# Performance work log

Measured on AMD Instinct MI355X. Metric: run time of the kernel, lower is better.

## Reference

```python
import jax, jax.numpy as jnp
import numpy as np

H, W = 8, 64
HK, WK = 7, 11
N = H * W            # 512 tokens
C = 512              # embed_dim
HEADS = 8
HD = C // HEADS      # 64
SCALE = HD ** -0.5
B = 32


def build_local_mask():
    # Faithful port of the build() mask construction.
    m = np.ones([N, H + HK - 1, W + WK - 1], dtype=np.int32)
    for h in range(H):
        for w in range(W):
            m[h * W + w, h:h + HK, w:w + WK] = 0
    m = m[:, HK // 2:H + HK // 2, WK // 2:W + WK // 2].reshape(-1, N).astype(bool)
    mask = np.where(m, -1e30, 0.0).astype(np.float32)
    return jnp.asarray(mask.reshape(1, 1, N, N))


def setup_inputs() -> dict:
    key = jax.random.key(0)
    k1, k2, k3, k4 = jax.random.split(key, 4)
    return {
        "x": jax.random.normal(k1, (B, N, C), dtype=jnp.float32),
        "w_qkv": jax.random.normal(k2, (C, 3 * C), dtype=jnp.float32) * (C ** -0.5),
        "w_proj": jax.random.normal(k3, (C, C), dtype=jnp.float32) * (C ** -0.5),
        "b_proj": jax.random.normal(k4, (C,), dtype=jnp.float32) * 0.01,
        "mask": build_local_mask(),
    }


def reference(x, w_qkv, w_proj, b_proj, mask):
    b = x.shape[0]
    qkv = x @ w_qkv                                   # [B, N, 3C]
    qkv = qkv.reshape(b, N, 3, HEADS, HD)
    qkv = jnp.transpose(qkv, (2, 0, 3, 1, 4))          # [3, B, heads, N, hd]
    q, k, v = qkv[0], qkv[1], qkv[2]
    attn = jnp.einsum("bhnd,bhmd->bhnm", q * SCALE, k) + mask  # [B, heads, N, N]
    attn = jax.nn.softmax(attn, axis=-1)
    out = jnp.einsum("bhnm,bhmd->bhnd", attn, v)       # [B, heads, N, hd]
    out = jnp.transpose(out, (0, 2, 1, 3)).reshape(b, N, C)
    return out @ w_proj + b_proj
```

## Files before the change

kernel.cpp:

```cpp
#include <hip/hip_runtime.h>
#include <hip/hip_bf16.h>

typedef __attribute__((ext_vector_type(8))) __bf16 bf16x8;
typedef __attribute__((ext_vector_type(4))) float f32x4;

__device__ __forceinline__ unsigned short f2bf(float f) {
    unsigned int u = __float_as_uint(f);
    unsigned int r = u + 0x7FFFu + ((u >> 16) & 1u);
    return (unsigned short)(r >> 16);
}

__device__ __forceinline__ void async_copy16(const unsigned short* g, unsigned short* l) {
    __builtin_amdgcn_global_load_lds(
        (__attribute__((address_space(1))) void*)(g),
        (__attribute__((address_space(3))) void*)(l), 16, 0, 0);
}

__global__ __launch_bounds__(256) void cvt_f32_bf16(const float4* __restrict__ in,
                                                    uint4* __restrict__ out, int n8) {
    int i = blockIdx.x * blockDim.x + threadIdx.x;
    if (i >= n8) return;
    float4 a = in[2 * i], b = in[2 * i + 1];
    union { unsigned short s[8]; uint4 v; } r;
    r.s[0] = f2bf(a.x); r.s[1] = f2bf(a.y); r.s[2] = f2bf(a.z); r.s[3] = f2bf(a.w);
    r.s[4] = f2bf(b.x); r.s[5] = f2bf(b.y); r.s[6] = f2bf(b.z); r.s[7] = f2bf(b.w);
    out[i] = r.v;
}

__global__ __launch_bounds__(256) void transpose_cvt(const float* __restrict__ in,
                                                     unsigned short* __restrict__ out,
                                                     int R, int C) {
    __shared__ float tile[32][33];
    int c0 = blockIdx.x * 32, r0 = blockIdx.y * 32;
    int tx = threadIdx.x, ty = threadIdx.y;
    #pragma unroll
    for (int i = 0; i < 32; i += 8)
        tile[ty + i][tx] = in[(size_t)(r0 + ty + i) * C + c0 + tx];
    __syncthreads();
    #pragma unroll
    for (int i = 0; i < 32; i += 8)
        out[(size_t)(c0 + ty + i) * R + r0 + tx] = f2bf(tile[tx][ty + i]);
}

__device__ __forceinline__ void gemm_core_128(const unsigned short* __restrict__ A,
                                              const unsigned short* __restrict__ Bt,
                                              int K, int m0, int n0, f32x4 acc[4][4]) {
    __shared__ unsigned short As[128 * 64];
    __shared__ unsigned short Bs[128 * 64];
    const int lane = threadIdx.x & 63;
    const int wv   = threadIdx.x >> 6;
    const int wm = (wv >> 1) * 64, wn = (wv & 1) * 64;
    const int l15 = lane & 15, l16 = lane >> 4;

    f32x4 zz = {0.f, 0.f, 0.f, 0.f};
    #pragma unroll
    for (int i = 0; i < 4; ++i)
        #pragma unroll
        for (int j = 0; j < 4; ++j) acc[i][j] = zz;

    for (int k0 = 0; k0 < K; k0 += 64) {
        if (k0) __syncthreads();
        #pragma unroll
        for (int c = 0; c < 4; ++c) {
            int flat16 = c * 256 + (int)threadIdx.x;
            int r  = flat16 >> 3;
            int kk = (flat16 & 7) * 8;
            async_copy16(A  + (size_t)(m0 + r) * K + k0 + kk, As + flat16 * 8);
            async_copy16(Bt + (size_t)(n0 + r) * K + k0 + kk, Bs + flat16 * 8);
        }
        __syncthreads();
        #pragma unroll
        for (int kk = 0; kk < 64; kk += 32) {
            bf16x8 a[4], b[4];
            #pragma unroll
            for (int i = 0; i < 4; ++i)
                a[i] = *(const bf16x8*)(const void*)(As + (wm + i * 16 + l15) * 64 + kk + l16 * 8);
            #pragma unroll
            for (int i = 0; i < 4; ++i)
                b[i] = *(const bf16x8*)(const void*)(Bs + (wn + i * 16 + l15) * 64 + kk + l16 * 8);
            #pragma unroll
            for (int i = 0; i < 4; ++i)
                #pragma unroll
                for (int j = 0; j < 4; ++j)
                    acc[i][j] = __builtin_amdgcn_mfma_f32_16x16x32_bf16(a[i], b[j], acc[i][j], 0, 0, 0);
        }
    }
}

__global__ __launch_bounds__(256) void gemm_qkv(const unsigned short* __restrict__ xb,
                                                const unsigned short* __restrict__ wT,
                                                unsigned short* __restrict__ Qb,
                                                unsigned short* __restrict__ Kb,
                                                unsigned short* __restrict__ Vb) {
    f32x4 acc[4][4];
    int m0 = blockIdx.y * 128, n0 = blockIdx.x * 128;
    gemm_core_128(xb, wT, 512, m0, n0, acc);
    const int lane = threadIdx.x & 63, wv = threadIdx.x >> 6;
    const int wm = (wv >> 1) * 64, wn = (wv & 1) * 64;
    const int l15 = lane & 15, l16 = lane >> 4;
    #pragma unroll
    for (int j = 0; j < 4; ++j) {
        int col = n0 + wn + j * 16 + l15;
        int t = col >> 9;
        int within = col & 511;
        int h = within >> 6, d = within & 63;
        unsigned short* dst = (t == 0) ? Qb : (t == 1) ? Kb : Vb;
        float scl = (t == 0) ? 0.125f : 1.0f;
        #pragma unroll
        for (int i = 0; i < 4; ++i)
            #pragma unroll
            for (int e = 0; e < 4; ++e) {
                int row = m0 + wm + i * 16 + (l16 << 2) + e;
                int b = row >> 9, n = row & 511;
                dst[(((size_t)b * 8 + h) * 512 + n) * 64 + d] = f2bf(acc[i][j][e] * scl);
            }
    }
}

__global__ __launch_bounds__(256) void attn_kernel(const unsigned short* __restrict__ Qb,
                                                   const unsigned short* __restrict__ Kb,
                                                   const unsigned short* __restrict__ Vb,
                                                   unsigned short* __restrict__ Ob) {
    __shared__ unsigned short Ks[128 * 72];
    __shared__ unsigned short Vt[64 * 136];
    __shared__ unsigned short Ps[4 * 32 * 136];

    const int bh = blockIdx.x >> 2;
    const int qt = blockIdx.x & 3;
    const int lane = threadIdx.x & 63;
    const int wv = threadIdx.x >> 6;
    const int l15 = lane & 15, l16 = lane >> 4;
    const int b = bh >> 3, h = bh & 7;

    const unsigned short* Qp = Qb + (size_t)bh * 512 * 64;
    const unsigned short* Kp = Kb + (size_t)bh * 512 * 64;
    const unsigned short* Vp = Vb + (size_t)bh * 512 * 64;
    unsigned short* Pw = Ps + wv * 32 * 136;

    const int qrow0 = qt * 128 + wv * 32;

    bf16x8 aQ[2][2];
    #pragma unroll
    for (int mf = 0; mf < 2; ++mf)
        #pragma unroll
        for (int kf = 0; kf < 2; ++kf)
            aQ[mf][kf] = *(const bf16x8*)(const void*)(Qp + (size_t)(qrow0 + mf * 16 + l15) * 64 + kf * 32 + l16 * 8);

    f32x4 o[2][4];
    f32x4 zz = {0.f, 0.f, 0.f, 0.f};
    float mrow[2][4], lrow[2][4];
    #pragma unroll
    for (int mf = 0; mf < 2; ++mf) {
        #pragma unroll
        for (int df = 0; df < 4; ++df) o[mf][df] = zz;
        #pragma unroll
        for (int j = 0; j < 4; ++j) { mrow[mf][j] = -INFINITY; lrow[mf][j] = 0.f; }
    }

    for (int kt = 0; kt < 4; ++kt) {
        if (((kt > qt) ? (kt - qt) : (qt - kt)) >= 3) continue;
        __syncthreads();
        #pragma unroll
        for (int c = 0; c < 4; ++c) {
            int flat16 = c * 256 + (int)threadIdx.x;
            int key = flat16 >> 3, d = (flat16 & 7) * 8;
            *(uint4*)(Ks + key * 72 + d) = *(const uint4*)(Kp + (size_t)(kt * 128 + key) * 64 + d);
        }
        #pragma unroll
        for (int c = 0; c < 4; ++c) {
            int flat16 = c * 256 + (int)threadIdx.x;
            int key = flat16 & 127, dc = flat16 >> 7;
            union { uint4 v; unsigned short s[8]; } t;
            t.v = *(const uint4*)(Vp + (size_t)(kt * 128 + key) * 64 + dc * 8);
            #pragma unroll
            for (int e = 0; e < 8; ++e) Vt[(dc * 8 + e) * 136 + key] = t.s[e];
        }
        __syncthreads();

        f32x4 s[2][8];
        #pragma unroll
        for (int mf = 0; mf < 2; ++mf)
            #pragma unroll
            for (int nf = 0; nf < 8; ++nf) s[mf][nf] = zz;
        #pragma unroll
        for (int nf = 0; nf < 8; ++nf) {
            bf16x8 bk0 = *(const bf16x8*)(const void*)(Ks + (nf * 16 + l15) * 72 + 0  + l16 * 8);
            bf16x8 bk1 = *(const bf16x8*)(const void*)(Ks + (nf * 16 + l15) * 72 + 32 + l16 * 8);
            #pragma unroll
            for (int mf = 0; mf < 2; ++mf) {
                s[mf][nf] = __builtin_amdgcn_mfma_f32_16x16x32_bf16(aQ[mf][0], bk0, s[mf][nf], 0, 0, 0);
                s[mf][nf] = __builtin_amdgcn_mfma_f32_16x16x32_bf16(aQ[mf][1], bk1, s[mf][nf], 0, 0, 0);
            }
        }

        float tmax[2][4];
        #pragma unroll
        for (int mf = 0; mf < 2; ++mf)
            #pragma unroll
            for (int j = 0; j < 4; ++j) tmax[mf][j] = -INFINITY;
        #pragma unroll
        for (int mf = 0; mf < 2; ++mf)
            #pragma unroll
            for (int nf = 0; nf < 8; ++nf) {
                int key = kt * 128 + nf * 16 + l15;
                int kh = key >> 6, kw = key & 63;
                #pragma unroll
                for (int j = 0; j < 4; ++j) {
                    int q = qrow0 + mf * 16 + (l16 << 2) + j;
                    int qh = q >> 6, qw = q & 63;
                    int dh = qh - kh; dh = dh < 0 ? -dh : dh;
                    int dw = qw - kw; dw = dw < 0 ? -dw : dw;
                    float v = (dh <= 3 && dw <= 5) ? s[mf][nf][j] : -1e30f;
                    s[mf][nf][j] = v;
                    tmax[mf][j] = fmaxf(tmax[mf][j], v);
                }
            }
        #pragma unroll
        for (int mf = 0; mf < 2; ++mf)
            #pragma unroll
            for (int j = 0; j < 4; ++j) {
                float t = tmax[mf][j];
                t = fmaxf(t, __shfl_xor(t, 1));
                t = fmaxf(t, __shfl_xor(t, 2));
                t = fmaxf(t, __shfl_xor(t, 4));
                t = fmaxf(t, __shfl_xor(t, 8));
                tmax[mf][j] = t;
            }
        float fscale[2][4];
        #pragma unroll
        for (int mf = 0; mf < 2; ++mf)
            #pragma unroll
            for (int j = 0; j < 4; ++j) {
                float mnew = fmaxf(mrow[mf][j], tmax[mf][j]);
                fscale[mf][j] = __expf(mrow[mf][j] - mnew);
                mrow[mf][j] = mnew;
                lrow[mf][j] *= fscale[mf][j];
            }
        #pragma unroll
        for (int mf = 0; mf < 2; ++mf)
            #pragma unroll
            for (int df = 0; df < 4; ++df)
                #pragma unroll
                for (int j = 0; j < 4; ++j) o[mf][df][j] *= fscale[mf][j];

        #pragma unroll
        for (int mf = 0; mf < 2; ++mf) {
            float lsum[4] = {0.f, 0.f, 0.f, 0.f};
            #pragma unroll
            for (int nf = 0; nf < 8; ++nf) {
                #pragma unroll
                for (int j = 0; j < 4; ++j) {
                    float p = __expf(s[mf][nf][j] - mrow[mf][j]);
                    lsum[j] += p;
                    Pw[(mf * 16 + (l16 << 2) + j) * 136 + nf * 16 + l15] = f2bf(p);
                }
            }
            #pragma unroll
            for (int j = 0; j < 4; ++j) {
                float t = lsum[j];
                t += __shfl_xor(t, 1); t += __shfl_xor(t, 2);
                t += __shfl_xor(t, 4); t += __shfl_xor(t, 8);
                lrow[mf][j] += t;
            }
        }
        __syncthreads();

        #pragma unroll
        for (int kf = 0; kf < 4; ++kf) {
            bf16x8 aP[2];
            #pragma unroll
            for (int mf = 0; mf < 2; ++mf)
                aP[mf] = *(const bf16x8*)(const void*)(Pw + (mf * 16 + l15) * 136 + kf * 32 + l16 * 8);
            #pragma unroll
            for (int df = 0; df < 4; ++df) {
                bf16x8 bV = *(const bf16x8*)(const void*)(Vt + (df * 16 + l15) * 136 + kf * 32 + l16 * 8);
                #pragma unroll
                for (int mf = 0; mf < 2; ++mf)
                    o[mf][df] = __builtin_amdgcn_mfma_f32_16x16x32_bf16(aP[mf], bV, o[mf][df], 0, 0, 0);
            }
        }
    }

    #pragma unroll
    for (int mf = 0; mf < 2; ++mf)
        #pragma unroll
        for (int j = 0; j < 4; ++j) {
            float inv = 1.0f / lrow[mf][j];
            int q = qrow0 + mf * 16 + (l16 << 2) + j;
            size_t base = ((size_t)b * 512 + q) * 512 + h * 64;
            #pragma unroll
            for (int df = 0; df < 4; ++df)
                Ob[base + df * 16 + l15] = f2bf(o[mf][df][j] * inv);
        }
}

__global__ __launch_bounds__(256) void gemm_proj(const unsigned short* __restrict__ Ab,
                                                 const unsigned short* __restrict__ wT,
                                                 const float* __restrict__ bias,
                                                 float* __restrict__ out) {
    f32x4 acc[4][4];
    int m0 = blockIdx.y * 128, n0 = blockIdx.x * 128;
    gemm_core_128(Ab, wT, 512, m0, n0, acc);
    const int lane = threadIdx.x & 63, wv = threadIdx.x >> 6;
    const int wm = (wv >> 1) * 64, wn = (wv & 1) * 64;
    const int l15 = lane & 15, l16 = lane >> 4;
    #pragma unroll
    for (int j = 0; j < 4; ++j) {
        int col = n0 + wn + j * 16 + l15;
        float bb = bias[col];
        #pragma unroll
        for (int i = 0; i < 4; ++i)
            #pragma unroll
            for (int e = 0; e < 4; ++e) {
                int row = m0 + wm + i * 16 + (l16 << 2) + e;
                out[(size_t)row * 512 + col] = acc[i][j][e] + bb;
            }
    }
}

extern "C" void kernel_launch(void* const* d_in, const int* in_sizes, int n_in,
                              void* d_out, int out_size, void* d_ws, size_t ws_size,
                              hipStream_t stream) {
    const float* x      = (const float*)d_in[0];
    const float* w_qkv  = (const float*)d_in[1];
    const float* w_proj = (const float*)d_in[2];
    const float* b_proj = (const float*)d_in[3];
    float* out = (float*)d_out;

    char* ws = (char*)d_ws;
    unsigned short* xb     = (unsigned short*)(ws);
    unsigned short* wqkvT  = (unsigned short*)(ws + 16777216);
    unsigned short* wprojT = (unsigned short*)(ws + 18350080);
    unsigned short* Qb     = (unsigned short*)(ws + 18874368);
    unsigned short* Kb     = (unsigned short*)(ws + 35651584);
    unsigned short* Vb     = (unsigned short*)(ws + 52428800);
    unsigned short* Ob     = xb;

    cvt_f32_bf16<<<4096, 256, 0, stream>>>((const float4*)x, (uint4*)xb, 1048576);
    transpose_cvt<<<dim3(48, 16), dim3(32, 8), 0, stream>>>(w_qkv, wqkvT, 512, 1536);
    transpose_cvt<<<dim3(16, 16), dim3(32, 8), 0, stream>>>(w_proj, wprojT, 512, 512);
    gemm_qkv<<<dim3(12, 128), 256, 0, stream>>>(xb, wqkvT, Qb, Kb, Vb);
    attn_kernel<<<1024, 256, 0, stream>>>(Qb, Kb, Vb, Ob);
    gemm_proj<<<dim3(4, 128), 256, 0, stream>>>(Ob, wprojT, b_proj, out);
}
```

Before: 124.2 us.

## Restructure local attention into per-image-row key tiles with transposed S and dead-block skipping

The attention kernel now walks key tiles of one image row (64 keys) instead of 128-key tiles. It skips rows farther than 3 from the warp's query row, and skips 16-key column groups that are fully outside the 11-wide window. S is computed transposed (K as the A operand) so each lane owns one query column. This lets the window mask be precomputed as a per-lane bitmask and cuts the row reductions to two cross-lane shuffles. P is packed with v_cvt_pk_bf16_f32 into per-wave LDS, the block barrier before PV is replaced by a compiler fence, LDS is reduced, and occupancy is hinted at 4 blocks per CU. The risks are per-wave LDS ordering subtleties and extra shuffles to redistribute the rescale factors.

```diff
diff --git a/kernel.cpp b/kernel.cpp
--- a/kernel.cpp
+++ b/kernel.cpp
@@ -117,181 +117,189 @@
     }
 }
 
-__global__ __launch_bounds__(256) void attn_kernel(const unsigned short* __restrict__ Qb,
-                                                   const unsigned short* __restrict__ Kb,
-                                                   const unsigned short* __restrict__ Vb,
-                                                   unsigned short* __restrict__ Ob) {
-    __shared__ unsigned short Ks[128 * 72];
-    __shared__ unsigned short Vt[64 * 136];
-    __shared__ unsigned short Ps[4 * 32 * 136];
+__global__ __launch_bounds__(256, 4) void attn_kernel(const unsigned short* __restrict__ Qb,
+                                                      const unsigned short* __restrict__ Kb,
+                                                      const unsigned short* __restrict__ Vb,
+                                                      unsigned short* __restrict__ Ob) {
+    __shared__ unsigned short Ks[64 * 72];
+    __shared__ unsigned short Vt[64 * 72];
+    __shared__ unsigned short Ps[4 * 32 * 72];
 
     const int bh = blockIdx.x >> 2;
     const int qt = blockIdx.x & 3;
-    const int lane = threadIdx.x & 63;
-    const int wv = threadIdx.x >> 6;
+    const int tid = threadIdx.x;
+    const int lane = tid & 63;
+    const int wv = tid >> 6;
     const int l15 = lane & 15, l16 = lane >> 4;
     const int b = bh >> 3, h = bh & 7;
 
     const unsigned short* Qp = Qb + (size_t)bh * 512 * 64;
     const unsigned short* Kp = Kb + (size_t)bh * 512 * 64;
     const unsigned short* Vp = Vb + (size_t)bh * 512 * 64;
-    unsigned short* Pw = Ps + wv * 32 * 136;
+    unsigned short* Pw = Ps + wv * 32 * 72;
 
     const int qrow0 = qt * 128 + wv * 32;
-
-    bf16x8 aQ[2][2];
-    #pragma unroll
-    for (int mf = 0; mf < 2; ++mf)
+    const int qh = qrow0 >> 6;
+    const int wq0 = qrow0 & 63;
+    const int dead_g = wq0 ? 0 : 3;
+
+    unsigned int wbits = 0;
+    {
+        int qw[2] = { wq0 + l15, wq0 + 16 + l15 };
+        #pragma unroll
+        for (int qf = 0; qf < 2; ++qf)
+            #pragma unroll
+            for (int g = 0; g < 4; ++g)
+                #pragma unroll
+                for (int j = 0; j < 4; ++j) {
+                    int kw = g * 16 + (l16 << 2) + j;
+                    int dw = qw[qf] - kw; dw = dw < 0 ? -dw : dw;
+                    wbits |= (dw <= 5 ? 1u : 0u) << (qf * 16 + g * 4 + j);
+                }
+    }
+
+    bf16x8 bQ[2][2];
+    #pragma unroll
+    for (int qf = 0; qf < 2; ++qf)
         #pragma unroll
         for (int kf = 0; kf < 2; ++kf)
-            aQ[mf][kf] = *(const bf16x8*)(const void*)(Qp + (size_t)(qrow0 + mf * 16 + l15) * 64 + kf * 32 + l16 * 8);
+            bQ[qf][kf] = *(const bf16x8*)(const void*)(Qp + (size_t)(qrow0 + qf * 16 + l15) * 64 + kf * 32 + l16 * 8);
 
     f32x4 o[2][4];
     f32x4 zz = {0.f, 0.f, 0.f, 0.f};
-    float mrow[2][4], lrow[2][4];
-    #pragma unroll
-    for (int mf = 0; mf < 2; ++mf) {
-        #pragma unroll
-        for (int df = 0; df < 4; ++df) o[mf][df] = zz;
-        #pragma unroll
-        for (int j = 0; j < 4; ++j) { mrow[mf][j] = -INFINITY; lrow[mf][j] = 0.f; }
-    }
-
-    for (int kt = 0; kt < 4; ++kt) {
-        if (((kt > qt) ? (kt - qt) : (qt - kt)) >= 3) continue;
+    float mrow[2] = {-INFINITY, -INFINITY}, lrow[2] = {0.f, 0.f};
+    #pragma unroll
+    for (int qf = 0; qf < 2; ++qf)
+        #pragma unroll
+        for (int df = 0; df < 4; ++df) o[qf][df] = zz;
+
+    for (int kh = 0; kh < 8; ++kh) {
+        int dlo = kh - 2 * qt;
+        if (dlo < -3 || dlo > 4) continue;
         __syncthreads();
         #pragma unroll
-        for (int c = 0; c < 4; ++c) {
-            int flat16 = c * 256 + (int)threadIdx.x;
-            int key = flat16 >> 3, d = (flat16 & 7) * 8;
-            *(uint4*)(Ks + key * 72 + d) = *(const uint4*)(Kp + (size_t)(kt * 128 + key) * 64 + d);
-        }
-        #pragma unroll
-        for (int c = 0; c < 4; ++c) {
-            int flat16 = c * 256 + (int)threadIdx.x;
-            int key = flat16 & 127, dc = flat16 >> 7;
+        for (int c = 0; c < 2; ++c) {
+            int flat16 = c * 256 + tid;
+            int key = flat16 >> 3, dk = (flat16 & 7) * 8;
+            *(uint4*)(void*)(Ks + key * 72 + dk) = *(const uint4*)(const void*)(Kp + ((size_t)(kh * 64 + key) * 64 + dk));
+        }
+        #pragma unroll
+        for (int c = 0; c < 2; ++c) {
+            int flat16 = c * 256 + tid;
+            int key = flat16 & 63, d8 = flat16 >> 6;
             union { uint4 v; unsigned short s[8]; } t;
-            t.v = *(const uint4*)(Vp + (size_t)(kt * 128 + key) * 64 + dc * 8);
-            #pragma unroll
-            for (int e = 0; e < 8; ++e) Vt[(dc * 8 + e) * 136 + key] = t.s[e];
+            t.v = *(const uint4*)(const void*)(Vp + ((size_t)(kh * 64 + key) * 64 + d8 * 8));
+            #pragma unroll
+            for (int e = 0; e < 8; ++e) Vt[(d8 * 8 + e) * 72 + key] = t.s[e];
         }
         __syncthreads();
 
-        f32x4 s[2][8];
-        #pragma unroll
-        for (int mf = 0; mf < 2; ++mf)
-            #pragma unroll
-            for (int nf = 0; nf < 8; ++nf) s[mf][nf] = zz;
-        #pragma unroll
-        for (int nf = 0; nf < 8; ++nf) {
-            bf16x8 bk0 = *(const bf16x8*)(const void*)(Ks + (nf * 16 + l15) * 72 + 0  + l16 * 8);
-            bf16x8 bk1 = *(const bf16x8*)(const void*)(Ks + (nf * 16 + l15) * 72 + 32 + l16 * 8);
-            #pragma unroll
-            for (int mf = 0; mf < 2; ++mf) {
-                s[mf][nf] = __builtin_amdgcn_mfma_f32_16x16x32_bf16(aQ[mf][0], bk0, s[mf][nf], 0, 0, 0);
-                s[mf][nf] = __builtin_amdgcn_mfma_f32_16x16x32_bf16(aQ[mf][1], bk1, s[mf][nf], 0, 0, 0);
-            }
-        }
-
-        float tmax[2][4];
-        #pragma unroll
-        for (int mf = 0; mf < 2; ++mf)
-            #pragma unroll
-            for (int j = 0; j < 4; ++j) tmax[mf][j] = -INFINITY;
-        #pragma unroll
-        for (int mf = 0; mf < 2; ++mf)
-            #pragma unroll
-            for (int nf = 0; nf < 8; ++nf) {
-                int key = kt * 128 + nf * 16 + l15;
-                int kh = key >> 6, kw = key & 63;
+        int adq = qh - kh; adq = adq < 0 ? -adq : adq;
+        if (adq > 3) continue;
+
+        f32x4 s[2][4];
+        #pragma unroll
+        for (int qf = 0; qf < 2; ++qf)
+            #pragma unroll
+            for (int g = 0; g < 4; ++g) s[qf][g] = zz;
+        #pragma unroll
+        for (int g = 0; g < 4; ++g) {
+            if (g == dead_g) continue;
+            bf16x8 aK0 = *(const bf16x8*)(const void*)(Ks + (g * 16 + l15) * 72 + 0  + l16 * 8);
+            bf16x8 aK1 = *(const bf16x8*)(const void*)(Ks + (g * 16 + l15) * 72 + 32 + l16 * 8);
+            #pragma unroll
+            for (int qf = 0; qf < 2; ++qf) {
+                s[qf][g] = __builtin_amdgcn_mfma_f32_16x16x32_bf16(aK0, bQ[qf][0], s[qf][g], 0, 0, 0);
+                s[qf][g] = __builtin_amdgcn_mfma_f32_16x16x32_bf16(aK1, bQ[qf][1], s[qf][g], 0, 0, 0);
+            }
+        }
+
+        float tmax[2] = {-1e30f, -1e30f};
+        #pragma unroll
+        for (int qf = 0; qf < 2; ++qf) {
+            #pragma unroll
+            for (int g = 0; g < 4; ++g) {
+                if (g == dead_g) continue;
                 #pragma unroll
                 for (int j = 0; j < 4; ++j) {
-                    int q = qrow0 + mf * 16 + (l16 << 2) + j;
-                    int qh = q >> 6, qw = q & 63;
-                    int dh = qh - kh; dh = dh < 0 ? -dh : dh;
-                    int dw = qw - kw; dw = dw < 0 ? -dw : dw;
-                    float v = (dh <= 3 && dw <= 5) ? s[mf][nf][j] : -1e30f;
-                    s[mf][nf][j] = v;
-                    tmax[mf][j] = fmaxf(tmax[mf][j], v);
+                    float v = ((wbits >> (qf * 16 + g * 4 + j)) & 1u) ? s[qf][g][j] : -1e30f;
+                    s[qf][g][j] = v;
+                    tmax[qf] = fmaxf(tmax[qf], v);
                 }
             }
-        #pragma unroll
-        for (int mf = 0; mf < 2; ++mf)
+            float t = tmax[qf];
+            t = fmaxf(t, __shfl_xor(t, 16));
+            t = fmaxf(t, __shfl_xor(t, 32));
+            tmax[qf] = t;
+        }
+
+        #pragma unroll
+        for (int qf = 0; qf < 2; ++qf) {
+            float mnew = fmaxf(mrow[qf], tmax[qf]);
+            float fs = __expf(mrow[qf] - mnew);
+            mrow[qf] = mnew;
+            lrow[qf] *= fs;
             #pragma unroll
             for (int j = 0; j < 4; ++j) {
-                float t = tmax[mf][j];
-                t = fmaxf(t, __shfl_xor(t, 1));
-                t = fmaxf(t, __shfl_xor(t, 2));
-                t = fmaxf(t, __shfl_xor(t, 4));
-                t = fmaxf(t, __shfl_xor(t, 8));
-                tmax[mf][j] = t;
-            }
-        float fscale[2][4];
-        #pragma unroll
-        for (int mf = 0; mf < 2; ++mf)
-            #pragma unroll
-            for (int j = 0; j < 4; ++j) {
-                float mnew = fmaxf(mrow[mf][j], tmax[mf][j]);
-                fscale[mf][j] = __expf(mrow[mf][j] - mnew);
-                mrow[mf][j] = mnew;
-                lrow[mf][j] *= fscale[mf][j];
-            }
-        #pragma unroll
-        for (int mf = 0; mf < 2; ++mf)
+                float fso = __shfl(fs, (l16 << 2) + j);
+                #pragma unroll
+                for (int df = 0; df < 4; ++df) o[qf][df][j] *= fso;
+            }
+        }
+
+        #pragma unroll
+        for (int qf = 0; qf < 2; ++qf) {
+            float lsum = 0.f;
+            #pragma unroll
+            for (int g = 0; g < 4; ++g) {
+                unsigned int lo, hi;
+                if (g == dead_g) {
+                    lo = 0u; hi = 0u;
+                } else {
+                    float e0 = __expf(s[qf][g][0] - mrow[qf]);
+                    float e1 = __expf(s[qf][g][1] - mrow[qf]);
+                    float e2 = __expf(s[qf][g][2] - mrow[qf]);
+                    float e3 = __expf(s[qf][g][3] - mrow[qf]);
+                    lsum += (e0 + e1) + (e2 + e3);
+                    asm("v_cvt_pk_bf16_f32 %0, %1, %2" : "=v"(lo) : "v"(e0), "v"(e1));
+                    asm("v_cvt_pk_bf16_f32 %0, %1, %2" : "=v"(hi) : "v"(e2), "v"(e3));
+                }
+                uint2 w; w.x = lo; w.y = hi;
+                *(uint2*)(void*)(Pw + (qf * 16 + l15) * 72 + g * 16 + (l16 << 2)) = w;
+            }
+            float t = lsum;
+            t += __shfl_xor(t, 16);
+            t += __shfl_xor(t, 32);
+            lrow[qf] += t;
+        }
+        asm volatile("" ::: "memory");
+
+        #pragma unroll
+        for (int kf = 0; kf < 2; ++kf) {
+            bf16x8 aP0 = *(const bf16x8*)(const void*)(Pw + (0 * 16 + l15) * 72 + kf * 32 + l16 * 8);
+            bf16x8 aP1 = *(const bf16x8*)(const void*)(Pw + (1 * 16 + l15) * 72 + kf * 32 + l16 * 8);
+            #pragma unroll
+            for (int df = 0; df < 4; ++df) {
+                bf16x8 bV = *(const bf16x8*)(const void*)(Vt + (df * 16 + l15) * 72 + kf * 32 + l16 * 8);
+                o[0][df] = __builtin_amdgcn_mfma_f32_16x16x32_bf16(aP0, bV, o[0][df], 0, 0, 0);
+                o[1][df] = __builtin_amdgcn_mfma_f32_16x16x32_bf16(aP1, bV, o[1][df], 0, 0, 0);
+            }
+        }
+    }
+
+    #pragma unroll
+    for (int qf = 0; qf < 2; ++qf) {
+        float linv = 1.0f / lrow[qf];
+        #pragma unroll
+        for (int j = 0; j < 4; ++j) {
+            float lj = __shfl(linv, (l16 << 2) + j);
+            int q = qrow0 + qf * 16 + (l16 << 2) + j;
+            size_t base = ((size_t)b * 512 + q) * 512 + h * 64;
             #pragma unroll
             for (int df = 0; df < 4; ++df)
-                #pragma unroll
-                for (int j = 0; j < 4; ++j) o[mf][df][j] *= fscale[mf][j];
-
-        #pragma unroll
-        for (int mf = 0; mf < 2; ++mf) {
-            float lsum[4] = {0.f, 0.f, 0.f, 0.f};
-            #pragma unroll
-            for (int nf = 0; nf < 8; ++nf) {
-                #pragma unroll
-                for (int j = 0; j < 4; ++j) {
-                    float p = __expf(s[mf][nf][j] - mrow[mf][j]);
-                    lsum[j] += p;
-                    Pw[(mf * 16 + (l16 << 2) + j) * 136 + nf * 16 + l15] = f2bf(p);
-                }
-            }
-            #pragma unroll
-            for (int j = 0; j < 4; ++j) {
-                float t = lsum[j];
-                t += __shfl_xor(t, 1); t += __shfl_xor(t, 2);
-                t += __shfl_xor(t, 4); t += __shfl_xor(t, 8);
-                lrow[mf][j] += t;
-            }
-        }
-        __syncthreads();
-
-        #pragma unroll
-        for (int kf = 0; kf < 4; ++kf) {
-            bf16x8 aP[2];
-            #pragma unroll
-            for (int mf = 0; mf < 2; ++mf)
-                aP[mf] = *(const bf16x8*)(const void*)(Pw + (mf * 16 + l15) * 136 + kf * 32 + l16 * 8);
-            #pragma unroll
-            for (int df = 0; df < 4; ++df) {
-                bf16x8 bV = *(const bf16x8*)(const void*)(Vt + (df * 16 + l15) * 136 + kf * 32 + l16 * 8);
-                #pragma unroll
-                for (int mf = 0; mf < 2; ++mf)
-                    o[mf][df] = __builtin_amdgcn_mfma_f32_16x16x32_bf16(aP[mf], bV, o[mf][df], 0, 0, 0);
-            }
-        }
-    }
-
-    #pragma unroll
-    for (int mf = 0; mf < 2; ++mf)
-        #pragma unroll
-        for (int j = 0; j < 4; ++j) {
-            float inv = 1.0f / lrow[mf][j];
-            int q = qrow0 + mf * 16 + (l16 << 2) + j;
-            size_t base = ((size_t)b * 512 + q) * 512 + h * 64;
-            #pragma unroll
-            for (int df = 0; df < 4; ++df)
-                Ob[base + df * 16 + l15] = f2bf(o[mf][df][j] * inv);
-        }
+                Ob[base + df * 16 + l15] = f2bf(o[qf][df][j] * lj);
+        }
+    }
 }
 
 __global__ __launch_bounds__(256) void gemm_proj(const unsigned short* __restrict__ Ab,
```

After: 104.3 us. -16.0%, faster.
